# Kernel optimization log

Measured on AMD Instinct MI355X. Metric: run time of the kernel, lower is better.

## Reference

```python
import jax, jax.numpy as jnp
import numpy as np

ALPHA = 1.702
LIMIT = 7.0

B, E = 128, 4          # tokens, top_k experts per token
N_EXPERTS = 32
K = 512                # d_model
C = 1024               # 2 * d_ff, interleaved glu/linear channels


def setup_inputs() -> dict:
    key = jax.random.key(0)
    k1, k2, k3, k4 = jax.random.split(key, 4)
    normed_x = jax.random.normal(k1, (B, K), dtype=jnp.float32)
    expert_indices = jax.random.randint(k2, (B, E), 0, N_EXPERTS, dtype=jnp.int32)
    mlp1_weight = jax.random.normal(k3, (N_EXPERTS, C, K), dtype=jnp.float32) * 0.02
    mlp1_bias = jax.random.normal(k4, (N_EXPERTS, C), dtype=jnp.float32) * 0.02
    return {
        "normed_x": normed_x,
        "expert_indices": expert_indices,
        "mlp1_weight": mlp1_weight,
        "mlp1_bias": mlp1_bias,
    }


def reference(normed_x, expert_indices, mlp1_weight, mlp1_bias):
    # Gather per-token expert weights/biases: [B,E,C,K] and [B,E,C]
    w = mlp1_weight[expert_indices]
    b = mlp1_bias[expert_indices]
    # Per-token batched matmul: t[b,e,c] = sum_k w[b,e,c,k] * x[b,k]
    t = jnp.einsum('beck,bk->bec', w, normed_x) + b
    # Interleaved split into gated / linear halves
    x_glu = jnp.minimum(t[..., ::2], LIMIT)               # clamp max only
    x_linear = jnp.clip(t[..., 1::2], -LIMIT, LIMIT)      # clamp both sides
    out_glu = x_glu * jax.nn.sigmoid(ALPHA * x_glu)
    return out_glu * (x_linear + 1.0)                     # [B, E, C//2]
```

## Files before the change

kernel.cpp:

```cpp
#include <hip/hip_runtime.h>
#include <hip/hip_bf16.h>

#define B_TOK   128
#define E_TOP   4
#define NEXP    32
#define KDIM    512
#define CDIM    1024
#define PAIRS   (B_TOK * E_TOP)
#define HALF_C  (CDIM / 2)

#define ALPHA   1.702f
#define LIMIT   7.0f

#define TT      32
#define MAXIT   48
#define ITSTRIDE 32

typedef __attribute__((ext_vector_type(8))) short short8;
typedef __attribute__((ext_vector_type(4))) float f32x4;

#define WS_ITEMS  32768
#define WS_XPK    40960

__device__ __forceinline__ unsigned pk2(float a, float b) {
    union { __hip_bfloat16 h; unsigned short u; } ca, cb;
    ca.h = __float2bfloat16(a);
    cb.h = __float2bfloat16(b);
    return (unsigned)ca.u | ((unsigned)cb.u << 16);
}

__device__ __forceinline__ short8 cvt8(float4 lo, float4 hi) {
    union { unsigned u[4]; short8 s; } r;
    r.u[0] = pk2(lo.x, lo.y);
    r.u[1] = pk2(lo.z, lo.w);
    r.u[2] = pk2(hi.x, hi.y);
    r.u[3] = pk2(hi.z, hi.w);
    return r.s;
}

__device__ __forceinline__ float glu_act(float g, float l) {
    g = fminf(g, LIMIT);
    l = fminf(fmaxf(l, -LIMIT), LIMIT);
    const float sg = 1.0f / (1.0f + __expf(-ALPHA * g));
    return (g * sg) * (l + 1.0f);
}

#define LDF4(p, off) (*(const float4*)((p) + (off)))

__global__ void prep_kernel(const float* __restrict__ x,
                            uint4* __restrict__ xpk,
                            const int* __restrict__ idx,
                            unsigned short* __restrict__ lists,
                            int* __restrict__ itemE,
                            int* __restrict__ itemB,
                            int* __restrict__ itemN,
                            int* __restrict__ nItems) {
    if (blockIdx.x != 0) {
        const int i = (blockIdx.x - 1) * 256 + threadIdx.x;
        const float4 a = LDF4(x, i * 8);
        const float4 b = LDF4(x, i * 8 + 4);
        uint4 r;
        r.x = pk2(a.x, a.y); r.y = pk2(a.z, a.w);
        r.z = pk2(b.x, b.y); r.w = pk2(b.z, b.w);
        xpk[i] = r;
        return;
    }
    __shared__ int cnt[NEXP];
    const int t = threadIdx.x;
    if (t < NEXP) cnt[t] = 0;
    __syncthreads();
    #pragma unroll
    for (int r = 0; r < 2; ++r) {
        const int p = t + r * 256;
        const int e = idx[p];
        const int pos = atomicAdd(&cnt[e], 1);
        lists[e * PAIRS + pos] = (unsigned short)p;
    }
    __syncthreads();
    if (t == 0) {
        int n = 0;
        for (int ee = 0; ee < NEXP; ++ee) {
            const int c = cnt[ee];
            for (int b = 0; b < c; b += TT) {
                itemE[n] = ee;
                itemB[n] = b;
                itemN[n] = min(TT, c - b);
                ++n;
            }
        }
        *nItems = n;
    }
}

__global__ __launch_bounds__(256, 4) void moe_mlp1_kernel(
    const float* __restrict__ w,
    const float* __restrict__ bias,
    const char* __restrict__ xpk,
    const unsigned short* __restrict__ lists,
    const int* __restrict__ itemE,
    const int* __restrict__ itemB,
    const int* __restrict__ itemN,
    const int* __restrict__ nItems,
    float* __restrict__ out)
{
    __shared__ char  xbl[32 * 1024];
    __shared__ float red[2][64][8];

    const int nI = *nItems;
    const int tid  = threadIdx.x;
    const int wv   = tid >> 6;
    const int lane = tid & 63;
    const int kh   = wv >> 1;
    const int cs   = wv & 1;
    const int kg   = lane >> 4;
    const int c16  = lane & 15;
    const int tA   = lane & 15;
    const int cBase = blockIdx.x * 32;

    for (int it = blockIdx.y; it < nI; it += ITSTRIDE) {
        if (it != (int)blockIdx.y) __syncthreads();

        const int e     = itemE[it];
        const int tBase = itemB[it];
        const int nT    = itemN[it];

        const int pr0 = (tA < nT)      ? (int)lists[e * PAIRS + tBase + tA]      : -1;
        const int pr1 = (tA + 16 < nT) ? (int)lists[e * PAIRS + tBase + tA + 16] : -1;
        const int rfb = (int)lists[e * PAIRS + tBase] >> 2;
        const int rr0 = (pr0 >= 0) ? (pr0 >> 2) : rfb;
        const int rr1 = (pr1 >= 0) ? (pr1 >> 2) : rfb;

        #pragma unroll
        for (int j = 0; j < 8; ++j) {
            const int f   = wv * 8 + j;
            const int s   = f >> 1;
            const int hlf = f & 1;
            const char* src = xpk + (size_t)(hlf ? rr1 : rr0) * 1024 + s * 64 + kg * 16;
            __builtin_amdgcn_global_load_lds(
                (const __attribute__((address_space(1))) void*)src,
                (__attribute__((address_space(3))) void*)&xbl[f * 1024],
                16, 0, 0);
        }

        const float4 bv = *(const float4*)(bias + (size_t)e * CDIM + cBase
                                           + cs * 16 + kg * 4);

        __syncthreads();

        const float* wp = w + ((size_t)e * CDIM + cBase + cs * 16 + c16) * KDIM
                            + kh * 256 + kg * 8;
        float4 w0[8], w1[8];
        #pragma unroll
        for (int p = 0; p < 8; ++p) {
            w0[p] = LDF4(wp, p * 32);
            w1[p] = LDF4(wp, p * 32 + 4);
        }

        f32x4 acc0 = {0.f, 0.f, 0.f, 0.f};
        f32x4 acc1 = {0.f, 0.f, 0.f, 0.f};
        const char* xb = &xbl[(kh * 8) * 2048 + lane * 16];

        #pragma unroll
        for (int s = 0; s < 8; ++s) {
            const short8 a  = cvt8(w0[s], w1[s]);
            const short8 b0 = *(const short8*)(xb + s * 2048);
            const short8 b1 = *(const short8*)(xb + s * 2048 + 1024);
            acc0 = __builtin_amdgcn_mfma_f32_16x16x32_bf16(a, b0, acc0, 0, 0, 0);
            acc1 = __builtin_amdgcn_mfma_f32_16x16x32_bf16(a, b1, acc1, 0, 0, 0);
        }

        if (kh == 1) {
            #pragma unroll
            for (int i = 0; i < 4; ++i) {
                red[cs][lane][i]     = acc0[i];
                red[cs][lane][4 + i] = acc1[i];
            }
        }
        __syncthreads();
        if (kh == 0) {
            #pragma unroll
            for (int i = 0; i < 4; ++i) {
                acc0[i] += red[cs][lane][i];
                acc1[i] += red[cs][lane][4 + i];
            }
            const int cb = cBase + cs * 16 + kg * 4;
            if (pr0 >= 0) {
                float2 o;
                o.x = glu_act(acc0[0] + bv.x, acc0[1] + bv.y);
                o.y = glu_act(acc0[2] + bv.z, acc0[3] + bv.w);
                *(float2*)&out[(size_t)pr0 * HALF_C + (cb >> 1)] = o;
            }
            if (pr1 >= 0) {
                float2 o;
                o.x = glu_act(acc1[0] + bv.x, acc1[1] + bv.y);
                o.y = glu_act(acc1[2] + bv.z, acc1[3] + bv.w);
                *(float2*)&out[(size_t)pr1 * HALF_C + (cb >> 1)] = o;
            }
        }
    }
}

extern "C" void kernel_launch(void* const* d_in, const int* in_sizes, int n_in,
                              void* d_out, int out_size, void* d_ws, size_t ws_size,
                              hipStream_t stream) {
    const float* x    = (const float*)d_in[0];
    const int*   idx  = (const int*)d_in[1];
    const float* w    = (const float*)d_in[2];
    const float* bias = (const float*)d_in[3];
    float* out = (float*)d_out;

    char* wsb = (char*)d_ws;
    unsigned short* lists = (unsigned short*)wsb;
    int* itemE  = (int*)(wsb + WS_ITEMS);
    int* itemB  = (int*)(wsb + WS_ITEMS + MAXIT * 4);
    int* itemN  = (int*)(wsb + WS_ITEMS + MAXIT * 8);
    int* nItems = (int*)(wsb + WS_ITEMS + MAXIT * 12);
    char* xpk   = wsb + WS_XPK;

    prep_kernel<<<33, 256, 0, stream>>>(x, (uint4*)xpk, idx, lists,
                                        itemE, itemB, itemN, nItems);

    dim3 grid(CDIM / 32, ITSTRIDE);
    moe_mlp1_kernel<<<grid, 256, 0, stream>>>(w, bias, xpk, lists,
                                              itemE, itemB, itemN, nItems, out);
}
```

Baseline: 25.12 us.

## Fuse routing and x conversion into the main kernel, one block row per expert

Removes the separate prep kernel. Each block now builds its own expert's token list in shared memory from the routing indices, and loads and converts x rows to bf16 into LDS itself. The grid maps one y-index per expert and loops over 32-token chunks, which removes one launch and the global workspace round trip. In exchange, every block rescans all 512 indices and redoes the fp32-to-bf16 conversion of x through registers instead of using async global-to-LDS copies. Load is also uneven across experts.

```diff
diff --git a/kernel.cpp b/kernel.cpp
--- a/kernel.cpp
+++ b/kernel.cpp
@@ -12,15 +12,8 @@
 #define ALPHA   1.702f
 #define LIMIT   7.0f
 
-#define TT      32
-#define MAXIT   48
-#define ITSTRIDE 32
-
 typedef __attribute__((ext_vector_type(8))) short short8;
 typedef __attribute__((ext_vector_type(4))) float f32x4;
-
-#define WS_ITEMS  32768
-#define WS_XPK    40960
 
 __device__ __forceinline__ unsigned pk2(float a, float b) {
     union { __hip_bfloat16 h; unsigned short u; } ca, cb;
@@ -47,108 +40,75 @@
 
 #define LDF4(p, off) (*(const float4*)((p) + (off)))
 
-__global__ void prep_kernel(const float* __restrict__ x,
-                            uint4* __restrict__ xpk,
-                            const int* __restrict__ idx,
-                            unsigned short* __restrict__ lists,
-                            int* __restrict__ itemE,
-                            int* __restrict__ itemB,
-                            int* __restrict__ itemN,
-                            int* __restrict__ nItems) {
-    if (blockIdx.x != 0) {
-        const int i = (blockIdx.x - 1) * 256 + threadIdx.x;
-        const float4 a = LDF4(x, i * 8);
-        const float4 b = LDF4(x, i * 8 + 4);
-        uint4 r;
-        r.x = pk2(a.x, a.y); r.y = pk2(a.z, a.w);
-        r.z = pk2(b.x, b.y); r.w = pk2(b.z, b.w);
-        xpk[i] = r;
-        return;
-    }
-    __shared__ int cnt[NEXP];
-    const int t = threadIdx.x;
-    if (t < NEXP) cnt[t] = 0;
-    __syncthreads();
-    #pragma unroll
-    for (int r = 0; r < 2; ++r) {
-        const int p = t + r * 256;
-        const int e = idx[p];
-        const int pos = atomicAdd(&cnt[e], 1);
-        lists[e * PAIRS + pos] = (unsigned short)p;
-    }
-    __syncthreads();
-    if (t == 0) {
-        int n = 0;
-        for (int ee = 0; ee < NEXP; ++ee) {
-            const int c = cnt[ee];
-            for (int b = 0; b < c; b += TT) {
-                itemE[n] = ee;
-                itemB[n] = b;
-                itemN[n] = min(TT, c - b);
-                ++n;
-            }
-        }
-        *nItems = n;
-    }
-}
-
 __global__ __launch_bounds__(256, 4) void moe_mlp1_kernel(
+    const float* __restrict__ x,
+    const int* __restrict__ idx,
     const float* __restrict__ w,
     const float* __restrict__ bias,
-    const char* __restrict__ xpk,
-    const unsigned short* __restrict__ lists,
-    const int* __restrict__ itemE,
-    const int* __restrict__ itemB,
-    const int* __restrict__ itemN,
-    const int* __restrict__ nItems,
     float* __restrict__ out)
 {
     __shared__ char  xbl[32 * 1024];
     __shared__ float red[2][64][8];
+    __shared__ unsigned short list[PAIRS];
+    __shared__ int cnt;
 
-    const int nI = *nItems;
-    const int tid  = threadIdx.x;
-    const int wv   = tid >> 6;
-    const int lane = tid & 63;
-    const int kh   = wv >> 1;
-    const int cs   = wv & 1;
-    const int kg   = lane >> 4;
-    const int c16  = lane & 15;
-    const int tA   = lane & 15;
+    const int e     = blockIdx.y;
     const int cBase = blockIdx.x * 32;
+    const int tid   = threadIdx.x;
+    const int wv    = tid >> 6;
+    const int lane  = tid & 63;
+    const int kh    = wv >> 1;
+    const int cs    = wv & 1;
+    const int kg    = lane >> 4;
+    const int c16   = lane & 15;
+    const int tA    = lane & 15;
 
-    for (int it = blockIdx.y; it < nI; it += ITSTRIDE) {
-        if (it != (int)blockIdx.y) __syncthreads();
+    if (tid == 0) cnt = 0;
+    __syncthreads();
+    #pragma unroll
+    for (int r = 0; r < 2; ++r) {
+        const int p = tid + r * 256;
+        if (idx[p] == e) {
+            const int pos = atomicAdd(&cnt, 1);
+            list[pos] = (unsigned short)p;
+        }
+    }
+    __syncthreads();
+    const int T = cnt;
 
-        const int e     = itemE[it];
-        const int tBase = itemB[it];
-        const int nT    = itemN[it];
+    const float* wp = w + ((size_t)e * CDIM + cBase + cs * 16 + c16) * KDIM
+                        + kh * 256 + kg * 8;
+    const float4 bv = *(const float4*)(bias + (size_t)e * CDIM + cBase
+                                       + cs * 16 + kg * 4);
+    const int cb = cBase + cs * 16 + kg * 4;
 
-        const int pr0 = (tA < nT)      ? (int)lists[e * PAIRS + tBase + tA]      : -1;
-        const int pr1 = (tA + 16 < nT) ? (int)lists[e * PAIRS + tBase + tA + 16] : -1;
-        const int rfb = (int)lists[e * PAIRS + tBase] >> 2;
-        const int rr0 = (pr0 >= 0) ? (pr0 >> 2) : rfb;
-        const int rr1 = (pr1 >= 0) ? (pr1 >> 2) : rfb;
+    for (int tb = 0; tb < T; tb += 32) {
+        if (tb) __syncthreads();
+        const int nT = min(32, T - tb);
 
         #pragma unroll
-        for (int j = 0; j < 8; ++j) {
-            const int f   = wv * 8 + j;
-            const int s   = f >> 1;
-            const int hlf = f & 1;
-            const char* src = xpk + (size_t)(hlf ? rr1 : rr0) * 1024 + s * 64 + kg * 16;
-            __builtin_amdgcn_global_load_lds(
-                (const __attribute__((address_space(1))) void*)src,
-                (__attribute__((address_space(3))) void*)&xbl[f * 1024],
-                16, 0, 0);
+        for (int r = 0; r < 2; ++r) {
+            const int u = tid + r * 256;
+            const int t = u & 31;
+            const int s = u >> 5;
+            const int pr = (int)list[tb + ((t < nT) ? t : 0)];
+            const float* xr = x + (size_t)(pr >> 2) * KDIM + s * 32;
+            const float4 f0 = LDF4(xr, 0),  f1 = LDF4(xr, 4);
+            const float4 f2 = LDF4(xr, 8),  f3 = LDF4(xr, 12);
+            const float4 f4 = LDF4(xr, 16), f5 = LDF4(xr, 20);
+            const float4 f6 = LDF4(xr, 24), f7 = LDF4(xr, 28);
+            char* db = &xbl[(s * 2 + (t >> 4)) * 1024 + (t & 15) * 16];
+            *(short8*)(db + 0 * 256) = cvt8(f0, f1);
+            *(short8*)(db + 1 * 256) = cvt8(f2, f3);
+            *(short8*)(db + 2 * 256) = cvt8(f4, f5);
+            *(short8*)(db + 3 * 256) = cvt8(f6, f7);
         }
 
-        const float4 bv = *(const float4*)(bias + (size_t)e * CDIM + cBase
-                                           + cs * 16 + kg * 4);
+        const int pr0 = (tA < nT)      ? (int)list[tb + tA]      : -1;
+        const int pr1 = (tA + 16 < nT) ? (int)list[tb + tA + 16] : -1;
 
         __syncthreads();
 
-        const float* wp = w + ((size_t)e * CDIM + cBase + cs * 16 + c16) * KDIM
-                            + kh * 256 + kg * 8;
         float4 w0[8], w1[8];
         #pragma unroll
         for (int p = 0; p < 8; ++p) {
@@ -183,7 +143,6 @@
                 acc0[i] += red[cs][lane][i];
                 acc1[i] += red[cs][lane][4 + i];
             }
-            const int cb = cBase + cs * 16 + kg * 4;
             if (pr0 >= 0) {
                 float2 o;
                 o.x = glu_act(acc0[0] + bv.x, acc0[1] + bv.y);
@@ -209,18 +168,6 @@
     const float* bias = (const float*)d_in[3];
     float* out = (float*)d_out;
 
-    char* wsb = (char*)d_ws;
-    unsigned short* lists = (unsigned short*)wsb;
-    int* itemE  = (int*)(wsb + WS_ITEMS);
-    int* itemB  = (int*)(wsb + WS_ITEMS + MAXIT * 4);
-    int* itemN  = (int*)(wsb + WS_ITEMS + MAXIT * 8);
-    int* nItems = (int*)(wsb + WS_ITEMS + MAXIT * 12);
-    char* xpk   = wsb + WS_XPK;
-
-    prep_kernel<<<33, 256, 0, stream>>>(x, (uint4*)xpk, idx, lists,
-                                        itemE, itemB, itemN, nItems);
-
-    dim3 grid(CDIM / 32, ITSTRIDE);
-    moe_mlp1_kernel<<<grid, 256, 0, stream>>>(w, bias, xpk, lists,
-                                              itemE, itemB, itemN, nItems, out);
+    dim3 grid(CDIM / 32, NEXP);
+    moe_mlp1_kernel<<<grid, 256, 0, stream>>>(x, idx, w, bias, out);
 }
```

After: 20.67 us. -17.7%, faster.
